# Kernel tuning notes

Hardware: AMD Instinct MI355X
Metric: run time of the kernel (lower is better)

The kernel has to match this reference:

```python
import jax, jax.numpy as jnp
import numpy as np

B, T, I, H = 128, 2048, 64, 128


def setup_inputs() -> dict:
    key = jax.random.key(0)
    ks = jax.random.split(key, 7)
    return {
        "input_data": jax.random.normal(ks[0], (B, T, I), dtype=jnp.float32),
        "h0": jax.random.normal(ks[1], (B, H), dtype=jnp.float32),
        "c0": jax.random.normal(ks[2], (B, H), dtype=jnp.float32),
        "W_ih": jax.random.normal(ks[3], (4 * H, I), dtype=jnp.float32) * 0.05,
        "W_hh": jax.random.normal(ks[4], (4 * H, H), dtype=jnp.float32) * 0.05,
        "b_ih": jax.random.normal(ks[5], (4 * H,), dtype=jnp.float32) * 0.05,
        "b_hh": jax.random.normal(ks[6], (4 * H,), dtype=jnp.float32) * 0.05,
    }


def reference(input_data, h0, c0, W_ih, W_hh, b_ih, b_hh):
    # Precompute input projections for all timesteps: [B, T, 4H]
    x_proj = jnp.einsum('bti,gi->btg', input_data, W_ih) + b_ih + b_hh

    def step(carry, xg):
        h, c = carry                      # [B, H]
        gates = xg + h @ W_hh.T           # [B, 4H]
        i_g, f_g, g_g, o_g = jnp.split(gates, 4, axis=-1)  # PyTorch order i,f,g,o
        i_g = jax.nn.sigmoid(i_g)
        f_g = jax.nn.sigmoid(f_g)
        g_g = jnp.tanh(g_g)
        o_g = jax.nn.sigmoid(o_g)
        c_new = f_g * c + i_g * g_g
        h_new = o_g * jnp.tanh(c_new)
        return (h_new, c_new), h_new

    (h_last, c_last), hs = jax.lax.scan(step, (h0, c0), jnp.swapaxes(x_proj, 0, 1))
    input_encoded = jnp.swapaxes(hs, 0, 1)  # [B, T, H]
    return (h_last[None], input_encoded)
```

## Files before the change

### kernel.cpp

```cpp
#include <hip/hip_runtime.h>

#define BB 128
#define TT 2048
#define II 64
#define HH 128
#define KK 192

typedef _Float16 h2 __attribute__((ext_vector_type(2)));
typedef _Float16 f16x8 __attribute__((ext_vector_type(8)));
typedef float f32x4 __attribute__((ext_vector_type(4)));

__device__ __forceinline__ h2 mkh2(float a, float b) {
    h2 r; r.x = (_Float16)a; r.y = (_Float16)b; return r;
}

__device__ __forceinline__ float rcp_fast(float x) {
    return __builtin_amdgcn_rcpf(x);
}

__device__ __forceinline__ float tanh_fast(float x) {
    return fmaf(rcp_fast(1.0f + __expf(-2.0f * x)), 2.0f, -1.0f);
}

__device__ __forceinline__ float sigmoid_fast(float x) {
    return rcp_fast(1.0f + __expf(-x));
}

__global__ __launch_bounds__(512, 2) void lstm_fused_kernel(
    const float* __restrict__ input,
    const float* __restrict__ h0,
    const float* __restrict__ c0,
    const float* __restrict__ W_ih,
    const float* __restrict__ W_hh,
    const float* __restrict__ b_ih,
    const float* __restrict__ b_hh,
    float* __restrict__ out)
{
    __shared__ __align__(16) h2 s_xh[2][KK / 2];

    const int tid  = threadIdx.x;
    const int b    = blockIdx.x;
    const int lane = tid & 63;
    const int w    = tid >> 6;
    const int grp  = lane >> 4;
    const int m    = lane & 15;
    const int r    = lane & 3;
    const int jb   = (w << 4) | (grp << 2);
    const int jown = jb | r;

    f16x8 wf[4][6];
#pragma unroll
    for (int g = 0; g < 4; ++g) {
        const int row = (g << 7) | (w << 4) | m;
#pragma unroll
        for (int kt = 0; kt < 6; ++kt) {
            const int k0 = 32 * kt + 8 * grp;
            const float* src = (k0 < II) ? (W_ih + row * II + k0)
                                         : (W_hh + row * HH + (k0 - II));
            const float4 v0 = reinterpret_cast<const float4*>(src)[0];
            const float4 v1 = reinterpret_cast<const float4*>(src)[1];
            f16x8 f;
            f[0] = (_Float16)v0.x; f[1] = (_Float16)v0.y;
            f[2] = (_Float16)v0.z; f[3] = (_Float16)v0.w;
            f[4] = (_Float16)v1.x; f[5] = (_Float16)v1.y;
            f[6] = (_Float16)v1.z; f[7] = (_Float16)v1.w;
            wf[g][kt] = f;
        }
    }

    f32x4 biasf[4];
#pragma unroll
    for (int g = 0; g < 4; ++g) {
#pragma unroll
        for (int rr = 0; rr < 4; ++rr) {
            const int row = (g << 7) | (jb + rr);
            biasf[g][rr] = b_ih[row] + b_hh[row];
        }
    }

    float c = c0[(size_t)b * HH + jown];
    if (tid < 64) {
        float2 hv = reinterpret_cast<const float2*>(h0 + (size_t)b * HH)[tid];
        s_xh[0][32 + tid] = mkh2(hv.x, hv.y);
    }

    const float2* xin = reinterpret_cast<const float2*>(input) + (size_t)b * TT * 32 + tid;
    float2 xb0, xb1, xb2, xb3;
    if (tid < 32) {
        xb0 = xin[(size_t)0 * 32];
        xb1 = xin[(size_t)1 * 32];
        xb2 = xin[(size_t)2 * 32];
        xb3 = xin[(size_t)3 * 32];
        s_xh[0][tid] = mkh2(xb0.x, xb0.y);
        xb0 = xin[(size_t)4 * 32];
    }
    __syncthreads();

    float* out_h = out;
    float* out_e = out + BB * HH;
    float hlast = 0.0f;
    const bool writer = (lane & 12) == 0;

    auto step = [&](int t, float2& xbn) {
        const int cb = t & 1, nb = cb ^ 1;

        if (tid < 32) {
            s_xh[nb][tid] = mkh2(xbn.x, xbn.y);
            int tn = t + 5; if (tn > TT - 1) tn = TT - 1;
            xbn = xin[(size_t)tn * 32];
        }

        const char* base = reinterpret_cast<const char*>(s_xh[cb]) + 16 * grp;
        f16x8 bf[6];
#pragma unroll
        for (int kt = 0; kt < 6; ++kt)
            bf[kt] = __builtin_bit_cast(f16x8,
                *reinterpret_cast<const uint4*>(base + 64 * kt));

        f32x4 acc0 = biasf[0], acc1 = biasf[1], acc2 = biasf[2], acc3 = biasf[3];
#pragma unroll
        for (int kt = 0; kt < 6; ++kt) {
            acc0 = __builtin_amdgcn_mfma_f32_16x16x32_f16(wf[0][kt], bf[kt], acc0, 0, 0, 0);
            acc1 = __builtin_amdgcn_mfma_f32_16x16x32_f16(wf[1][kt], bf[kt], acc1, 0, 0, 0);
            acc2 = __builtin_amdgcn_mfma_f32_16x16x32_f16(wf[2][kt], bf[kt], acc2, 0, 0, 0);
            acc3 = __builtin_amdgcn_mfma_f32_16x16x32_f16(wf[3][kt], bf[kt], acc3, 0, 0, 0);
        }

        const bool s1 = (lane & 1) != 0, s2 = (lane & 2) != 0;
        float p0 = s2 ? (s1 ? acc0[3] : acc0[2]) : (s1 ? acc0[1] : acc0[0]);
        float p1 = s2 ? (s1 ? acc1[3] : acc1[2]) : (s1 ? acc1[1] : acc1[0]);
        float p2 = s2 ? (s1 ? acc2[3] : acc2[2]) : (s1 ? acc2[1] : acc2[0]);
        float p3 = s2 ? (s1 ? acc3[3] : acc3[2]) : (s1 ? acc3[1] : acc3[0]);

        float ig = sigmoid_fast(p0);
        float fg = sigmoid_fast(p1);
        float gg = tanh_fast(p2);
        float og = sigmoid_fast(p3);

        c = fmaf(fg, c, ig * gg);
        float hv = og * tanh_fast(c);
        hlast = hv;

        if (writer) {
            reinterpret_cast<_Float16*>(s_xh[nb])[II + jown] = (_Float16)hv;
            out_e[((size_t)b * TT + t) * HH + jown] = hv;
        }

        __syncthreads();
    };

    for (int t0 = 0; t0 < TT; t0 += 4) {
        step(t0 + 0, xb1);
        step(t0 + 1, xb2);
        step(t0 + 2, xb3);
        step(t0 + 3, xb0);
    }

    if (writer) out_h[(size_t)b * HH + jown] = hlast;
}

extern "C" void kernel_launch(void* const* d_in, const int* in_sizes, int n_in,
                              void* d_out, int out_size, void* d_ws, size_t ws_size,
                              hipStream_t stream) {
    const float* input = (const float*)d_in[0];
    const float* h0    = (const float*)d_in[1];
    const float* c0    = (const float*)d_in[2];
    const float* W_ih  = (const float*)d_in[3];
    const float* W_hh  = (const float*)d_in[4];
    const float* b_ih  = (const float*)d_in[5];
    const float* b_hh  = (const float*)d_in[6];
    float* out = (float*)d_out;

    hipLaunchKernelGGL(lstm_fused_kernel, dim3(BB), dim3(512), 0, stream,
                       input, h0, c0, W_ih, W_hh, b_ih, b_hh, out);
}
```

Measured before the change: 1.293 ms.

## Precompute next step's input projection off the recurrent critical path

Splits the fused [x;h] MFMA chain into an input-projection part and a recurrent part. The W_ih·x MFMAs for step t+1 are issued after the recurrent MFMAs of step t, so they overlap with the activation math instead of lengthening the serial dependency chain. To support this, x staging uses a triple-buffered shared array with a deeper prefetch, and the bias is added per lane after extraction. The change adds register pressure and some index bookkeeping.

After: 1.383 ms. +6.9%, slower.

```diff
diff --git a/kernel.cpp b/kernel.cpp
--- a/kernel.cpp
+++ b/kernel.cpp
@@ -4,7 +4,6 @@
 #define TT 2048
 #define II 64
 #define HH 128
-#define KK 192
 
 typedef _Float16 h2 __attribute__((ext_vector_type(2)));
 typedef _Float16 f16x8 __attribute__((ext_vector_type(8)));
@@ -24,6 +23,10 @@
 
 __device__ __forceinline__ float sigmoid_fast(float x) {
     return rcp_fast(1.0f + __expf(-x));
+}
+
+__device__ __forceinline__ f16x8 ld_frag(const void* p) {
+    return __builtin_bit_cast(f16x8, *reinterpret_cast<const uint4*>(p));
 }
 
 __global__ __launch_bounds__(512, 2) void lstm_fused_kernel(
@@ -36,7 +39,8 @@
     const float* __restrict__ b_hh,
     float* __restrict__ out)
 {
-    __shared__ __align__(16) h2 s_xh[2][KK / 2];
+    __shared__ __align__(16) h2 s_x[3][II / 2];
+    __shared__ __align__(16) h2 s_h[2][HH / 2];
 
     const int tid  = threadIdx.x;
     const int b    = blockIdx.x;
@@ -45,18 +49,16 @@
     const int grp  = lane >> 4;
     const int m    = lane & 15;
     const int r    = lane & 3;
-    const int jb   = (w << 4) | (grp << 2);
-    const int jown = jb | r;
-
-    f16x8 wf[4][6];
+    const int jown = (w << 4) | (grp << 2) | r;
+
+    f16x8 wfx[4][2];
+    f16x8 wfh[4][4];
 #pragma unroll
     for (int g = 0; g < 4; ++g) {
         const int row = (g << 7) | (w << 4) | m;
 #pragma unroll
-        for (int kt = 0; kt < 6; ++kt) {
-            const int k0 = 32 * kt + 8 * grp;
-            const float* src = (k0 < II) ? (W_ih + row * II + k0)
-                                         : (W_hh + row * HH + (k0 - II));
+        for (int kt = 0; kt < 2; ++kt) {
+            const float* src = W_ih + row * II + 32 * kt + 8 * grp;
             const float4 v0 = reinterpret_cast<const float4*>(src)[0];
             const float4 v1 = reinterpret_cast<const float4*>(src)[1];
             f16x8 f;
@@ -64,24 +66,31 @@
             f[2] = (_Float16)v0.z; f[3] = (_Float16)v0.w;
             f[4] = (_Float16)v1.x; f[5] = (_Float16)v1.y;
             f[6] = (_Float16)v1.z; f[7] = (_Float16)v1.w;
-            wf[g][kt] = f;
-        }
-    }
-
-    f32x4 biasf[4];
-#pragma unroll
-    for (int g = 0; g < 4; ++g) {
-#pragma unroll
-        for (int rr = 0; rr < 4; ++rr) {
-            const int row = (g << 7) | (jb + rr);
-            biasf[g][rr] = b_ih[row] + b_hh[row];
-        }
-    }
+            wfx[g][kt] = f;
+        }
+#pragma unroll
+        for (int kt = 0; kt < 4; ++kt) {
+            const float* src = W_hh + row * HH + 32 * kt + 8 * grp;
+            const float4 v0 = reinterpret_cast<const float4*>(src)[0];
+            const float4 v1 = reinterpret_cast<const float4*>(src)[1];
+            f16x8 f;
+            f[0] = (_Float16)v0.x; f[1] = (_Float16)v0.y;
+            f[2] = (_Float16)v0.z; f[3] = (_Float16)v0.w;
+            f[4] = (_Float16)v1.x; f[5] = (_Float16)v1.y;
+            f[6] = (_Float16)v1.z; f[7] = (_Float16)v1.w;
+            wfh[g][kt] = f;
+        }
+    }
+
+    float bs[4];
+#pragma unroll
+    for (int g = 0; g < 4; ++g)
+        bs[g] = b_ih[(g << 7) | jown] + b_hh[(g << 7) | jown];
 
     float c = c0[(size_t)b * HH + jown];
     if (tid < 64) {
         float2 hv = reinterpret_cast<const float2*>(h0 + (size_t)b * HH)[tid];
-        s_xh[0][32 + tid] = mkh2(hv.x, hv.y);
+        s_h[0][tid] = mkh2(hv.x, hv.y);
     }
 
     const float2* xin = reinterpret_cast<const float2*>(input) + (size_t)b * TT * 32 + tid;
@@ -91,10 +100,24 @@
         xb1 = xin[(size_t)1 * 32];
         xb2 = xin[(size_t)2 * 32];
         xb3 = xin[(size_t)3 * 32];
-        s_xh[0][tid] = mkh2(xb0.x, xb0.y);
+        s_x[0][tid] = mkh2(xb0.x, xb0.y);
+        s_x[1][tid] = mkh2(xb1.x, xb1.y);
         xb0 = xin[(size_t)4 * 32];
+        xb1 = xin[(size_t)5 * 32];
     }
     __syncthreads();
+
+    f32x4 acc[4];
+    {
+        const char* xbp = reinterpret_cast<const char*>(s_x[0]) + 16 * grp;
+        f16x8 xf0 = ld_frag(xbp), xf1 = ld_frag(xbp + 64);
+#pragma unroll
+        for (int g = 0; g < 4; ++g) {
+            f32x4 z = {0.f, 0.f, 0.f, 0.f};
+            z = __builtin_amdgcn_mfma_f32_16x16x32_f16(wfx[g][0], xf0, z, 0, 0, 0);
+            acc[g] = __builtin_amdgcn_mfma_f32_16x16x32_f16(wfx[g][1], xf1, z, 0, 0, 0);
+        }
+    }
 
     float* out_h = out;
     float* out_e = out + BB * HH;
@@ -105,44 +128,57 @@
         const int cb = t & 1, nb = cb ^ 1;
 
         if (tid < 32) {
-            s_xh[nb][tid] = mkh2(xbn.x, xbn.y);
-            int tn = t + 5; if (tn > TT - 1) tn = TT - 1;
+            s_x[(t + 2) % 3][tid] = mkh2(xbn.x, xbn.y);
+            int tn = t + 6; if (tn > TT - 1) tn = TT - 1;
             xbn = xin[(size_t)tn * 32];
         }
 
-        const char* base = reinterpret_cast<const char*>(s_xh[cb]) + 16 * grp;
-        f16x8 bf[6];
-#pragma unroll
-        for (int kt = 0; kt < 6; ++kt)
-            bf[kt] = __builtin_bit_cast(f16x8,
-                *reinterpret_cast<const uint4*>(base + 64 * kt));
-
-        f32x4 acc0 = biasf[0], acc1 = biasf[1], acc2 = biasf[2], acc3 = biasf[3];
-#pragma unroll
-        for (int kt = 0; kt < 6; ++kt) {
-            acc0 = __builtin_amdgcn_mfma_f32_16x16x32_f16(wf[0][kt], bf[kt], acc0, 0, 0, 0);
-            acc1 = __builtin_amdgcn_mfma_f32_16x16x32_f16(wf[1][kt], bf[kt], acc1, 0, 0, 0);
-            acc2 = __builtin_amdgcn_mfma_f32_16x16x32_f16(wf[2][kt], bf[kt], acc2, 0, 0, 0);
-            acc3 = __builtin_amdgcn_mfma_f32_16x16x32_f16(wf[3][kt], bf[kt], acc3, 0, 0, 0);
-        }
+        const char* hb = reinterpret_cast<const char*>(s_h[cb]) + 16 * grp;
+        f16x8 hf0 = ld_frag(hb);
+        f16x8 hf1 = ld_frag(hb + 64);
+        f16x8 hf2 = ld_frag(hb + 128);
+        f16x8 hf3 = ld_frag(hb + 192);
+#pragma unroll
+        for (int g = 0; g < 4; ++g)
+            acc[g] = __builtin_amdgcn_mfma_f32_16x16x32_f16(wfh[g][0], hf0, acc[g], 0, 0, 0);
+#pragma unroll
+        for (int g = 0; g < 4; ++g)
+            acc[g] = __builtin_amdgcn_mfma_f32_16x16x32_f16(wfh[g][1], hf1, acc[g], 0, 0, 0);
+#pragma unroll
+        for (int g = 0; g < 4; ++g)
+            acc[g] = __builtin_amdgcn_mfma_f32_16x16x32_f16(wfh[g][2], hf2, acc[g], 0, 0, 0);
+#pragma unroll
+        for (int g = 0; g < 4; ++g)
+            acc[g] = __builtin_amdgcn_mfma_f32_16x16x32_f16(wfh[g][3], hf3, acc[g], 0, 0, 0);
 
         const bool s1 = (lane & 1) != 0, s2 = (lane & 2) != 0;
-        float p0 = s2 ? (s1 ? acc0[3] : acc0[2]) : (s1 ? acc0[1] : acc0[0]);
-        float p1 = s2 ? (s1 ? acc1[3] : acc1[2]) : (s1 ? acc1[1] : acc1[0]);
-        float p2 = s2 ? (s1 ? acc2[3] : acc2[2]) : (s1 ? acc2[1] : acc2[0]);
-        float p3 = s2 ? (s1 ? acc3[3] : acc3[2]) : (s1 ? acc3[1] : acc3[0]);
-
-        float ig = sigmoid_fast(p0);
-        float fg = sigmoid_fast(p1);
-        float gg = tanh_fast(p2);
-        float og = sigmoid_fast(p3);
+        float p0 = s2 ? (s1 ? acc[0][3] : acc[0][2]) : (s1 ? acc[0][1] : acc[0][0]);
+        float p1 = s2 ? (s1 ? acc[1][3] : acc[1][2]) : (s1 ? acc[1][1] : acc[1][0]);
+        float p2 = s2 ? (s1 ? acc[2][3] : acc[2][2]) : (s1 ? acc[2][1] : acc[2][0]);
+        float p3 = s2 ? (s1 ? acc[3][3] : acc[3][2]) : (s1 ? acc[3][1] : acc[3][0]);
+
+        {
+            const char* xbp = reinterpret_cast<const char*>(s_x[(t + 1) % 3]) + 16 * grp;
+            f16x8 xf0 = ld_frag(xbp), xf1 = ld_frag(xbp + 64);
+#pragma unroll
+            for (int g = 0; g < 4; ++g) {
+                f32x4 z = {0.f, 0.f, 0.f, 0.f};
+                z = __builtin_amdgcn_mfma_f32_16x16x32_f16(wfx[g][0], xf0, z, 0, 0, 0);
+                acc[g] = __builtin_amdgcn_mfma_f32_16x16x32_f16(wfx[g][1], xf1, z, 0, 0, 0);
+            }
+        }
+
+        float ig = sigmoid_fast(p0 + bs[0]);
+        float fg = sigmoid_fast(p1 + bs[1]);
+        float gg = tanh_fast(p2 + bs[2]);
+        float og = sigmoid_fast(p3 + bs[3]);
 
         c = fmaf(fg, c, ig * gg);
         float hv = og * tanh_fast(c);
         hlast = hv;
 
         if (writer) {
-            reinterpret_cast<_Float16*>(s_xh[nb])[II + jown] = (_Float16)hv;
+            reinterpret_cast<_Float16*>(s_h[nb])[jown] = (_Float16)hv;
             out_e[((size_t)b * TT + t) * HH + jown] = hv;
         }
 
@@ -150,10 +186,10 @@
     };
 
     for (int t0 = 0; t0 < TT; t0 += 4) {
-        step(t0 + 0, xb1);
-        step(t0 + 1, xb2);
-        step(t0 + 2, xb3);
-        step(t0 + 3, xb0);
+        step(t0 + 0, xb2);
+        step(t0 + 1, xb3);
+        step(t0 + 2, xb0);
+        step(t0 + 3, xb1);
     }
 
     if (writer) out_h[(size_t)b * HH + jown] = hlast;
```

## Split input projection into separate parallel kernel before recurrent LSTM loop

Applied to the files above, without the earlier changes.

Adds a fully parallel kernel that precomputes the input projection plus biases for every timestep into an fp16 workspace, so the serial recurrent kernel only multiplies by W_hh (4 instead of 6 MFMA k-tiles per step) and loads the precomputed gates with a two-step prefetch. This is meant to shorten the per-step critical path of the sequential loop. In exchange it adds a 256 MB workspace write and read, and the original fused kernel is kept as a fallback when the workspace is too small.

Result: slower. 1.435 ms (+11.0%).

```diff
diff --git a/kernel.cpp b/kernel.cpp
--- a/kernel.cpp
+++ b/kernel.cpp
@@ -4,7 +4,6 @@
 #define TT 2048
 #define II 64
 #define HH 128
-#define KK 192
 
 typedef _Float16 h2 __attribute__((ext_vector_type(2)));
 typedef _Float16 f16x8 __attribute__((ext_vector_type(8)));
@@ -14,6 +13,18 @@
     h2 r; r.x = (_Float16)a; r.y = (_Float16)b; return r;
 }
 
+__device__ __forceinline__ h2 u2h(unsigned u) {
+    return __builtin_bit_cast(h2, u);
+}
+
+__device__ __forceinline__ float fdot2f(h2 a, h2 b, float c) {
+#if __has_builtin(__builtin_amdgcn_fdot2)
+    return __builtin_amdgcn_fdot2(a, b, c, false);
+#else
+    return fmaf((float)a.y, (float)b.y, fmaf((float)a.x, (float)b.x, c));
+#endif
+}
+
 __device__ __forceinline__ float rcp_fast(float x) {
     return __builtin_amdgcn_rcpf(x);
 }
@@ -26,17 +37,90 @@
     return rcp_fast(1.0f + __expf(-x));
 }
 
-__global__ __launch_bounds__(512, 2) void lstm_fused_kernel(
+__device__ __forceinline__ f16x8 ld_frag(const void* p) {
+    return __builtin_bit_cast(f16x8, *reinterpret_cast<const uint4*>(p));
+}
+
+__global__ __launch_bounds__(512, 2) void xproj_kernel(
     const float* __restrict__ input,
+    const float* __restrict__ W_ih,
+    const float* __restrict__ b_ih,
+    const float* __restrict__ b_hh,
+    _Float16* __restrict__ xproj)
+{
+    __shared__ __align__(16) h2 sx[32][II / 2];
+
+    const int tid = threadIdx.x;
+    const int bt  = blockIdx.x;
+    const int b   = bt >> 6;
+    const int tt  = (bt & 63) << 5;
+
+    h2 wr[II / 2];
+    {
+        const float4* p = reinterpret_cast<const float4*>(W_ih + (size_t)tid * II);
+#pragma unroll
+        for (int q = 0; q < II / 4; ++q) {
+            float4 v = p[q];
+            wr[2 * q]     = mkh2(v.x, v.y);
+            wr[2 * q + 1] = mkh2(v.z, v.w);
+        }
+    }
+    const float bias = b_ih[tid] + b_hh[tid];
+
+    {
+        const int tl = tid >> 4, k4 = tid & 15;
+        float4 v = *reinterpret_cast<const float4*>(
+            input + ((size_t)b * TT + tt + tl) * II + 4 * k4);
+        h2* dst = &sx[tl][2 * k4];
+        dst[0] = mkh2(v.x, v.y);
+        dst[1] = mkh2(v.z, v.w);
+    }
+    __syncthreads();
+
+    _Float16* op = xproj + ((size_t)b * TT + tt) * 512 + tid;
+#pragma unroll 4
+    for (int tl = 0; tl < 32; ++tl) {
+        const uint4* xr = reinterpret_cast<const uint4*>(&sx[tl][0]);
+        float a0 = bias, a1 = 0.f, a2 = 0.f, a3 = 0.f;
+#pragma unroll
+        for (int q = 0; q < 8; ++q) {
+            uint4 v = xr[q];
+            a0 = fdot2f(wr[4 * q + 0], u2h(v.x), a0);
+            a1 = fdot2f(wr[4 * q + 1], u2h(v.y), a1);
+            a2 = fdot2f(wr[4 * q + 2], u2h(v.z), a2);
+            a3 = fdot2f(wr[4 * q + 3], u2h(v.w), a3);
+        }
+        op[(size_t)tl * 512] = (_Float16)((a0 + a1) + (a2 + a3));
+    }
+}
+
+struct XPF { uint2 q0, q1, q2, q3; };
+
+__device__ __forceinline__ XPF ldxp(const _Float16* xpb, int t, int jb) {
+    const char* p = reinterpret_cast<const char*>(xpb) + ((size_t)t * 512 + jb) * 2;
+    XPF r;
+    r.q0 = *reinterpret_cast<const uint2*>(p);
+    r.q1 = *reinterpret_cast<const uint2*>(p + 256);
+    r.q2 = *reinterpret_cast<const uint2*>(p + 512);
+    r.q3 = *reinterpret_cast<const uint2*>(p + 768);
+    return r;
+}
+
+__device__ __forceinline__ f32x4 cvtq(uint2 q) {
+    h2 a = __builtin_bit_cast(h2, q.x), b = __builtin_bit_cast(h2, q.y);
+    f32x4 r;
+    r[0] = (float)a.x; r[1] = (float)a.y; r[2] = (float)b.x; r[3] = (float)b.y;
+    return r;
+}
+
+__global__ __launch_bounds__(512, 2) void lstm_rec_kernel(
+    const _Float16* __restrict__ xproj,
     const float* __restrict__ h0,
     const float* __restrict__ c0,
-    const float* __restrict__ W_ih,
     const float* __restrict__ W_hh,
-    const float* __restrict__ b_ih,
-    const float* __restrict__ b_hh,
     float* __restrict__ out)
 {
-    __shared__ __align__(16) h2 s_xh[2][KK / 2];
+    __shared__ __align__(16) h2 s_h[2][HH / 2];
 
     const int tid  = threadIdx.x;
     const int b    = blockIdx.x;
@@ -48,15 +132,136 @@
     const int jb   = (w << 4) | (grp << 2);
     const int jown = jb | r;
 
-    f16x8 wf[4][6];
+    f16x8 wfh[4][4];
 #pragma unroll
     for (int g = 0; g < 4; ++g) {
         const int row = (g << 7) | (w << 4) | m;
 #pragma unroll
+        for (int kt = 0; kt < 4; ++kt) {
+            const float* src = W_hh + (size_t)row * HH + 32 * kt + 8 * grp;
+            const float4 v0 = reinterpret_cast<const float4*>(src)[0];
+            const float4 v1 = reinterpret_cast<const float4*>(src)[1];
+            f16x8 f;
+            f[0] = (_Float16)v0.x; f[1] = (_Float16)v0.y;
+            f[2] = (_Float16)v0.z; f[3] = (_Float16)v0.w;
+            f[4] = (_Float16)v1.x; f[5] = (_Float16)v1.y;
+            f[6] = (_Float16)v1.z; f[7] = (_Float16)v1.w;
+            wfh[g][kt] = f;
+        }
+    }
+
+    float c = c0[(size_t)b * HH + jown];
+    if (tid < 64) {
+        float2 hv = reinterpret_cast<const float2*>(h0 + (size_t)b * HH)[tid];
+        s_h[0][tid] = mkh2(hv.x, hv.y);
+    }
+
+    const _Float16* xpb = xproj + (size_t)b * TT * 512;
+    XPF xf0 = ldxp(xpb, 0, jb);
+    XPF xf1 = ldxp(xpb, 1, jb);
+    __syncthreads();
+
+    float* out_h = out;
+    float* out_e = out + BB * HH;
+    float hlast = 0.0f;
+    const bool writer = (lane & 12) == 0;
+
+    auto step = [&](int t, XPF& xp) {
+        const int cb = t & 1, nb = cb ^ 1;
+
+        const char* hb = reinterpret_cast<const char*>(s_h[cb]) + 16 * grp;
+        f16x8 hf0 = ld_frag(hb);
+        f16x8 hf1 = ld_frag(hb + 64);
+        f16x8 hf2 = ld_frag(hb + 128);
+        f16x8 hf3 = ld_frag(hb + 192);
+
+        f32x4 acc0 = cvtq(xp.q0);
+        f32x4 acc1 = cvtq(xp.q1);
+        f32x4 acc2 = cvtq(xp.q2);
+        f32x4 acc3 = cvtq(xp.q3);
+
+        {
+            int tn = t + 2; if (tn > TT - 1) tn = TT - 1;
+            xp = ldxp(xpb, tn, jb);
+        }
+
+        acc0 = __builtin_amdgcn_mfma_f32_16x16x32_f16(wfh[0][0], hf0, acc0, 0, 0, 0);
+        acc1 = __builtin_amdgcn_mfma_f32_16x16x32_f16(wfh[1][0], hf0, acc1, 0, 0, 0);
+        acc2 = __builtin_amdgcn_mfma_f32_16x16x32_f16(wfh[2][0], hf0, acc2, 0, 0, 0);
+        acc3 = __builtin_amdgcn_mfma_f32_16x16x32_f16(wfh[3][0], hf0, acc3, 0, 0, 0);
+        acc0 = __builtin_amdgcn_mfma_f32_16x16x32_f16(wfh[0][1], hf1, acc0, 0, 0, 0);
+        acc1 = __builtin_amdgcn_mfma_f32_16x16x32_f16(wfh[1][1], hf1, acc1, 0, 0, 0);
+        acc2 = __builtin_amdgcn_mfma_f32_16x16x32_f16(wfh[2][1], hf1, acc2, 0, 0, 0);
+        acc3 = __builtin_amdgcn_mfma_f32_16x16x32_f16(wfh[3][1], hf1, acc3, 0, 0, 0);
+        acc0 = __builtin_amdgcn_mfma_f32_16x16x32_f16(wfh[0][2], hf2, acc0, 0, 0, 0);
+        acc1 = __builtin_amdgcn_mfma_f32_16x16x32_f16(wfh[1][2], hf2, acc1, 0, 0, 0);
+        acc2 = __builtin_amdgcn_mfma_f32_16x16x32_f16(wfh[2][2], hf2, acc2, 0, 0, 0);
+        acc3 = __builtin_amdgcn_mfma_f32_16x16x32_f16(wfh[3][2], hf2, acc3, 0, 0, 0);
+        acc0 = __builtin_amdgcn_mfma_f32_16x16x32_f16(wfh[0][3], hf3, acc0, 0, 0, 0);
+        acc1 = __builtin_amdgcn_mfma_f32_16x16x32_f16(wfh[1][3], hf3, acc1, 0, 0, 0);
+        acc2 = __builtin_amdgcn_mfma_f32_16x16x32_f16(wfh[2][3], hf3, acc2, 0, 0, 0);
+        acc3 = __builtin_amdgcn_mfma_f32_16x16x32_f16(wfh[3][3], hf3, acc3, 0, 0, 0);
+
+        const bool s1 = (lane & 1) != 0, s2 = (lane & 2) != 0;
+        float p0 = s2 ? (s1 ? acc0[3] : acc0[2]) : (s1 ? acc0[1] : acc0[0]);
+        float p1 = s2 ? (s1 ? acc1[3] : acc1[2]) : (s1 ? acc1[1] : acc1[0]);
+        float p2 = s2 ? (s1 ? acc2[3] : acc2[2]) : (s1 ? acc2[1] : acc2[0]);
+        float p3 = s2 ? (s1 ? acc3[3] : acc3[2]) : (s1 ? acc3[1] : acc3[0]);
+
+        float ig = sigmoid_fast(p0);
+        float fg = sigmoid_fast(p1);
+        float gg = tanh_fast(p2);
+        float og = sigmoid_fast(p3);
+
+        c = fmaf(fg, c, ig * gg);
+        float hv = og * tanh_fast(c);
+        hlast = hv;
+
+        if (writer) {
+            reinterpret_cast<_Float16*>(s_h[nb])[jown] = (_Float16)hv;
+            out_e[((size_t)b * TT + t) * HH + jown] = hv;
+        }
+
+        __syncthreads();
+    };
+
+    for (int t0 = 0; t0 < TT; t0 += 4) {
+        step(t0 + 0, xf0);
+        step(t0 + 1, xf1);
+        step(t0 + 2, xf0);
+        step(t0 + 3, xf1);
+    }
+
+    if (writer) out_h[(size_t)b * HH + jown] = hlast;
+}
+
+__global__ __launch_bounds__(512, 2) void lstm_fused_kernel(
+    const float* __restrict__ input, const float* __restrict__ h0,
+    const float* __restrict__ c0, const float* __restrict__ W_ih,
+    const float* __restrict__ W_hh, const float* __restrict__ b_ih,
+    const float* __restrict__ b_hh, float* __restrict__ out)
+{
+    __shared__ __align__(16) h2 s_xh[2][96];
+
+    const int tid  = threadIdx.x;
+    const int b    = blockIdx.x;
+    const int lane = tid & 63;
+    const int w    = tid >> 6;
+    const int grp  = lane >> 4;
+    const int m    = lane & 15;
+    const int r    = lane & 3;
+    const int jb   = (w << 4) | (grp << 2);
+    const int jown = jb | r;
+
+    f16x8 wf[4][6];
+#pragma unroll
+    for (int g = 0; g < 4; ++g) {
+        const int row = (g << 7) | (w << 4) | m;
+#pragma unroll
         for (int kt = 0; kt < 6; ++kt) {
             const int k0 = 32 * kt + 8 * grp;
-            const float* src = (k0 < II) ? (W_ih + row * II + k0)
-                                         : (W_hh + row * HH + (k0 - II));
+            const float* src = (k0 < II) ? (W_ih + (size_t)row * II + k0)
+                                         : (W_hh + (size_t)row * HH + (k0 - II));
             const float4 v0 = reinterpret_cast<const float4*>(src)[0];
             const float4 v1 = reinterpret_cast<const float4*>(src)[1];
             f16x8 f;
@@ -70,13 +275,10 @@
 
     f32x4 biasf[4];
 #pragma unroll
-    for (int g = 0; g < 4; ++g) {
-#pragma unroll
-        for (int rr = 0; rr < 4; ++rr) {
-            const int row = (g << 7) | (jb + rr);
-            biasf[g][rr] = b_ih[row] + b_hh[row];
-        }
-    }
+    for (int g = 0; g < 4; ++g)
+#pragma unroll
+        for (int rr = 0; rr < 4; ++rr)
+            biasf[g][rr] = b_ih[(g << 7) | (jb + rr)] + b_hh[(g << 7) | (jb + rr)];
 
     float c = c0[(size_t)b * HH + jown];
     if (tid < 64) {
@@ -103,20 +305,16 @@
 
     auto step = [&](int t, float2& xbn) {
         const int cb = t & 1, nb = cb ^ 1;
-
         if (tid < 32) {
             s_xh[nb][tid] = mkh2(xbn.x, xbn.y);
             int tn = t + 5; if (tn > TT - 1) tn = TT - 1;
             xbn = xin[(size_t)tn * 32];
         }
-
         const char* base = reinterpret_cast<const char*>(s_xh[cb]) + 16 * grp;
         f16x8 bf[6];
 #pragma unroll
         for (int kt = 0; kt < 6; ++kt)
-            bf[kt] = __builtin_bit_cast(f16x8,
-                *reinterpret_cast<const uint4*>(base + 64 * kt));
-
+            bf[kt] = ld_frag(base + 64 * kt);
         f32x4 acc0 = biasf[0], acc1 = biasf[1], acc2 = biasf[2], acc3 = biasf[3];
 #pragma unroll
         for (int kt = 0; kt < 6; ++kt) {
@@ -125,27 +323,22 @@
             acc2 = __builtin_amdgcn_mfma_f32_16x16x32_f16(wf[2][kt], bf[kt], acc2, 0, 0, 0);
             acc3 = __builtin_amdgcn_mfma_f32_16x16x32_f16(wf[3][kt], bf[kt], acc3, 0, 0, 0);
         }
-
         const bool s1 = (lane & 1) != 0, s2 = (lane & 2) != 0;
         float p0 = s2 ? (s1 ? acc0[3] : acc0[2]) : (s1 ? acc0[1] : acc0[0]);
         float p1 = s2 ? (s1 ? acc1[3] : acc1[2]) : (s1 ? acc1[1] : acc1[0]);
         float p2 = s2 ? (s1 ? acc2[3] : acc2[2]) : (s1 ? acc2[1] : acc2[0]);
         float p3 = s2 ? (s1 ? acc3[3] : acc3[2]) : (s1 ? acc3[1] : acc3[0]);
-
         float ig = sigmoid_fast(p0);
         float fg = sigmoid_fast(p1);
         float gg = tanh_fast(p2);
         float og = sigmoid_fast(p3);
-
         c = fmaf(fg, c, ig * gg);
         float hv = og * tanh_fast(c);
         hlast = hv;
-
         if (writer) {
             reinterpret_cast<_Float16*>(s_xh[nb])[II + jown] = (_Float16)hv;
             out_e[((size_t)b * TT + t) * HH + jown] = hv;
         }
-
         __syncthreads();
     };
 
@@ -155,7 +348,6 @@
         step(t0 + 2, xb3);
         step(t0 + 3, xb0);
     }
-
     if (writer) out_h[(size_t)b * HH + jown] = hlast;
 }
 
@@ -171,6 +363,15 @@
     const float* b_hh  = (const float*)d_in[6];
     float* out = (float*)d_out;
 
-    hipLaunchKernelGGL(lstm_fused_kernel, dim3(BB), dim3(512), 0, stream,
-                       input, h0, c0, W_ih, W_hh, b_ih, b_hh, out);
-}
+    const size_t need = (size_t)BB * TT * 512 * sizeof(_Float16);
+    if (d_ws != nullptr && ws_size >= need) {
+        _Float16* xproj = (_Float16*)d_ws;
+        hipLaunchKernelGGL(xproj_kernel, dim3(BB * (TT / 32)), dim3(512), 0, stream,
+                           input, W_ih, b_ih, b_hh, xproj);
+        hipLaunchKernelGGL(lstm_rec_kernel, dim3(BB), dim3(512), 0, stream,
+                           xproj, h0, c0, W_hh, out);
+    } else {
+        hipLaunchKernelGGL(lstm_fused_kernel, dim3(BB), dim3(512), 0, stream,
+                           input, h0, c0, W_ih, W_hh, b_ih, b_hh, out);
+    }
+}
```
